# Kernel optimization log

Hardware: AMD Instinct MI355X
Metric: run time of the kernel (lower is better)

The kernel has to match this reference:

```python
import jax, jax.numpy as jnp
import numpy as np

GFD = 4096   # global feature dim (VGG fc7)
DH = 1024    # 2 * hidden_dim


def setup_inputs() -> dict:
    key = jax.random.key(0)
    ks = jax.random.split(key, 10)
    b, t_k = 32, 196
    s = lambda fan_in: 1.0 / np.sqrt(fan_in)
    return {
        "global_features": jax.random.normal(ks[0], (b, t_k, GFD), jnp.float32),
        "s_t_hat": jax.random.normal(ks[1], (b, DH), jnp.float32),
        "coverage_img": jnp.zeros((b, t_k, 1), jnp.float32),
        # params
        "Wg": jax.random.normal(ks[2], (GFD, GFD), jnp.float32) * s(GFD),
        "bg": jnp.zeros((GFD,), jnp.float32),
        "Gs": jax.random.normal(ks[3], (GFD, DH), jnp.float32) * s(GFD),
        "bgs": jnp.zeros((DH,), jnp.float32),
        "Wgs": jax.random.normal(ks[4], (DH, DH), jnp.float32) * s(DH),  # w_g_star, no bias
        "Wdec": jax.random.normal(ks[5], (DH, DH), jnp.float32) * s(DH),  # decode_proj
        "bdec": jnp.zeros((DH,), jnp.float32),
        "v": jax.random.normal(ks[6], (DH, 1), jnp.float32) * s(DH),  # score vector, no bias
    }


def reference(global_features, s_t_hat, coverage_img, Wg, bg, Gs, bgs, Wgs, Wdec, bdec, v):
    # g_star: project 4096-d region features -> 1024-d   [b, t_k, DH]
    g1 = global_features @ Wg + bg
    g_star = g1 @ Gs + bgs
    # additive (Bahdanau) scores with coverage
    w_g_star = g_star @ Wgs                       # [b, t_k, DH]
    dec_fea = s_t_hat @ Wdec + bdec               # [b, DH]
    e_a = jnp.tanh(w_g_star + dec_fea[:, None, :] + coverage_img)  # [b, t_k, DH]
    scores = e_a @ v                              # [b, t_k, 1]
    alpha_a = jax.nn.softmax(scores, axis=1)      # softmax over regions
    # attention-weighted context (the bmm)
    c_img = jnp.einsum("bt,btd->bd", alpha_a[..., 0], g_star)  # [b, DH]
    coverage_new = coverage_img + alpha_a
    return c_img, coverage_new, alpha_a
```

## Files before the change

kernel.cpp:

```cpp
#include <hip/hip_runtime.h>
#include <hip/hip_bf16.h>

typedef __attribute__((ext_vector_type(8))) short short8;
typedef __attribute__((ext_vector_type(4))) float floatx4;

#define GLOBAL_AS __attribute__((address_space(1)))
#define LDS_AS    __attribute__((address_space(3)))

__device__ __forceinline__ unsigned short f2bf_rne(float x) {
  unsigned int u = __float_as_uint(x);
  u += 0x7fffu + ((u >> 16) & 1u);
  return (unsigned short)(u >> 16);
}

__global__ void cast_f32_bf16_kernel(const float* __restrict__ in,
                                     unsigned short* __restrict__ out, int n8) {
  int i = blockIdx.x * 256 + threadIdx.x;
  if (i >= n8) return;
  const float4* p = (const float4*)in;
  float4 v0 = p[2 * i], v1 = p[2 * i + 1];
  short8 o;
  o[0] = (short)f2bf_rne(v0.x); o[1] = (short)f2bf_rne(v0.y);
  o[2] = (short)f2bf_rne(v0.z); o[3] = (short)f2bf_rne(v0.w);
  o[4] = (short)f2bf_rne(v1.x); o[5] = (short)f2bf_rne(v1.y);
  o[6] = (short)f2bf_rne(v1.z); o[7] = (short)f2bf_rne(v1.w);
  *(short8*)(out + 8 * (size_t)i) = o;
}

__global__ void transpose_cast_kernel(const float* __restrict__ in,
                                      unsigned short* __restrict__ out, int R, int C) {
  __shared__ unsigned short tile[32][33];
  int tx = threadIdx.x & 31, ty = threadIdx.x >> 5;
  int r0 = blockIdx.y * 32, c0 = blockIdx.x * 32;
#pragma unroll
  for (int j = 0; j < 32; j += 8)
    tile[ty + j][tx] = f2bf_rne(in[(size_t)(r0 + ty + j) * C + c0 + tx]);
  __syncthreads();
#pragma unroll
  for (int j = 0; j < 32; j += 8)
    out[(size_t)(c0 + ty + j) * R + r0 + tx] = tile[tx][ty + j];
}

__global__ void zero4_kernel(float* __restrict__ p, int n4) {
  int i = blockIdx.x * 256 + threadIdx.x;
  if (i < n4) ((float4*)p)[i] = make_float4(0.f, 0.f, 0.f, 0.f);
}
__global__ void init_vec_kernel(const float* __restrict__ src, float* __restrict__ dst) {
  int i = blockIdx.x * 256 + threadIdx.x;
  dst[i] = src[i];
}
__global__ void bias1_accum_kernel(const float* __restrict__ bg, const float* __restrict__ Gs,
                                   float* __restrict__ bias1) {
  int j = blockIdx.x * 256 + threadIdx.x;
  int k0 = blockIdx.y * 256;
  float acc = 0.f;
  for (int k = 0; k < 256; ++k) acc += bg[k0 + k] * Gs[(size_t)(k0 + k) * 1024 + j];
  atomicAdd(&bias1[j], acc);
}

__global__ void init_dec_kernel(const float* __restrict__ bdec, float* __restrict__ dec) {
  int i = blockIdx.x * 256 + threadIdx.x;
  dec[i] = bdec[i & 1023];
}
__global__ void dec_accum_kernel(const float* __restrict__ sth, const float* __restrict__ Wdec,
                                 float* __restrict__ dec) {
  __shared__ float ss[32][128];
  const int tid = threadIdx.x;
  const int k0 = blockIdx.y * 128;
  for (int i = tid; i < 32 * 128; i += 256) {
    int bb = i >> 7, kk = i & 127;
    ss[bb][kk] = sth[bb * 1024 + k0 + kk];
  }
  __syncthreads();
  const int j = blockIdx.x * 256 + tid;
  float acc[32];
#pragma unroll
  for (int b = 0; b < 32; ++b) acc[b] = 0.f;
  for (int kk = 0; kk < 128; ++kk) {
    float w = Wdec[(size_t)(k0 + kk) * 1024 + j];
#pragma unroll
    for (int b = 0; b < 32; ++b) acc[b] += ss[b][kk] * w;
  }
  for (int b = 0; b < 32; ++b) atomicAdd(&dec[b * 1024 + j], acc[b]);
}

template <int BM, int BN, bool HAS_BIAS, bool WRITE_F32, bool WRITE_BF16>
__global__ __launch_bounds__(256, 4) void gemm_tile_kernel(
    const unsigned short* __restrict__ A, const unsigned short* __restrict__ BT,
    const float* __restrict__ bias, float* __restrict__ Cf,
    unsigned short* __restrict__ Cb, int M, int N, int K) {
  constexpr int AF = BM / 32;
  constexpr int BF = BN / 32;
  __shared__ unsigned short lds_a[BM * 32];
  __shared__ unsigned short lds_b[BN * 32];
  const int tid = threadIdx.x;
  const int lane = tid & 63;
  const int wave = tid >> 6;
  const int wm = wave >> 1, wn = wave & 1;
  const int quad = lane >> 4, col = lane & 15;
  const int m0 = blockIdx.y * BM, n0 = blockIdx.x * BN;

  floatx4 acc[AF][BF] = {};

  const int srow = tid >> 2;
  const int skoff = (tid & 3) * 8;
  const unsigned short* a_ptr = A + (size_t)(m0 + srow) * K + skoff;
  const unsigned short* b_ptr = BT + (size_t)(n0 + srow) * K + skoff;
  const size_t rowskip = (size_t)64 * K;
  char* la_dst = (char*)lds_a + tid * 16;
  char* lb_dst = (char*)lds_b + tid * 16;

  for (int kt = 0; kt < K; kt += 32) {
    __syncthreads();
#pragma unroll
    for (int c = 0; c < BM / 64; ++c)
      __builtin_amdgcn_global_load_lds((const GLOBAL_AS void*)(a_ptr + c * rowskip),
                                       (LDS_AS void*)(la_dst + c * 4096), 16, 0, 0);
#pragma unroll
    for (int c = 0; c < BN / 64; ++c)
      __builtin_amdgcn_global_load_lds((const GLOBAL_AS void*)(b_ptr + c * rowskip),
                                       (LDS_AS void*)(lb_dst + c * 4096), 16, 0, 0);
    a_ptr += 32; b_ptr += 32;
    __syncthreads();
    short8 af[AF], bf[BF];
#pragma unroll
    for (int t = 0; t < AF; ++t)
      af[t] = *(const short8*)((const char*)lds_a + (wm * (BM / 2) + t * 16 + col) * 64 + quad * 16);
#pragma unroll
    for (int t = 0; t < BF; ++t)
      bf[t] = *(const short8*)((const char*)lds_b + (wn * (BN / 2) + t * 16 + col) * 64 + quad * 16);
#pragma unroll
    for (int tm = 0; tm < AF; ++tm)
#pragma unroll
      for (int tn = 0; tn < BF; ++tn)
        acc[tm][tn] = __builtin_amdgcn_mfma_f32_16x16x32_bf16(af[tm], bf[tn], acc[tm][tn], 0, 0, 0);
  }

#pragma unroll
  for (int tm = 0; tm < AF; ++tm) {
    const int mg = m0 + wm * (BM / 2) + tm * 16 + quad * 4;
#pragma unroll
    for (int tn = 0; tn < BF; ++tn) {
      const int ng = n0 + wn * (BN / 2) + tn * 16 + col;
      const float bv = HAS_BIAS ? bias[ng] : 0.0f;
#pragma unroll
      for (int r = 0; r < 4; ++r) {
        const float val = acc[tm][tn][r] + bv;
        if (WRITE_F32) Cf[(size_t)(mg + r) * N + ng] = val;
        if (WRITE_BF16) Cb[(size_t)(mg + r) * N + ng] = f2bf_rne(val);
      }
    }
  }
}

__global__ __launch_bounds__(256, 4) void gemm_scores_kernel(
    const unsigned short* __restrict__ A, const unsigned short* __restrict__ BT,
    const float* __restrict__ dec, const float* __restrict__ cov,
    const float* __restrict__ v, float* __restrict__ scores, int M, int N, int K) {
  __shared__ unsigned short lds_a[128 * 32];
  __shared__ unsigned short lds_b[64 * 32];
  const int tid = threadIdx.x;
  const int lane = tid & 63;
  const int wave = tid >> 6;
  const int wm = wave >> 1, wn = wave & 1;
  const int quad = lane >> 4, col = lane & 15;
  const int m0 = blockIdx.y * 128, n0 = blockIdx.x * 64;

  floatx4 acc[4][2] = {};

  const int srow = tid >> 2;
  const int skoff = (tid & 3) * 8;
  const unsigned short* a_ptr = A + (size_t)(m0 + srow) * K + skoff;
  const unsigned short* b_ptr = BT + (size_t)(n0 + srow) * K + skoff;
  const size_t rowskip = (size_t)64 * K;
  char* la_dst = (char*)lds_a + tid * 16;
  char* lb_dst = (char*)lds_b + tid * 16;

  for (int kt = 0; kt < K; kt += 32) {
    __syncthreads();
    __builtin_amdgcn_global_load_lds((const GLOBAL_AS void*)(a_ptr), (LDS_AS void*)(la_dst), 16, 0, 0);
    __builtin_amdgcn_global_load_lds((const GLOBAL_AS void*)(a_ptr + rowskip), (LDS_AS void*)(la_dst + 4096), 16, 0, 0);
    __builtin_amdgcn_global_load_lds((const GLOBAL_AS void*)(b_ptr), (LDS_AS void*)(lb_dst), 16, 0, 0);
    a_ptr += 32; b_ptr += 32;
    __syncthreads();
    short8 af[4], bf[2];
#pragma unroll
    for (int t = 0; t < 4; ++t)
      af[t] = *(const short8*)((const char*)lds_a + (wm * 64 + t * 16 + col) * 64 + quad * 16);
#pragma unroll
    for (int t = 0; t < 2; ++t)
      bf[t] = *(const short8*)((const char*)lds_b + (wn * 32 + t * 16 + col) * 64 + quad * 16);
#pragma unroll
    for (int tm = 0; tm < 4; ++tm)
#pragma unroll
      for (int tn = 0; tn < 2; ++tn)
        acc[tm][tn] = __builtin_amdgcn_mfma_f32_16x16x32_bf16(af[tm], bf[tn], acc[tm][tn], 0, 0, 0);
  }

  const int n_base = n0 + wn * 32;
  float vv[2];
#pragma unroll
  for (int tn = 0; tn < 2; ++tn) vv[tn] = v[n_base + tn * 16 + col];
#pragma unroll
  for (int tm = 0; tm < 4; ++tm) {
#pragma unroll
    for (int r = 0; r < 4; ++r) {
      const int row = m0 + wm * 64 + tm * 16 + quad * 4 + r;
      const int b = row / 196;
      const float cw = cov[row];
      const float* dr = dec + b * 1024 + n_base;
      float s = 0.f;
#pragma unroll
      for (int tn = 0; tn < 2; ++tn)
        s += tanhf(acc[tm][tn][r] + dr[tn * 16 + col] + cw) * vv[tn];
      s += __shfl_xor(s, 1, 64);
      s += __shfl_xor(s, 2, 64);
      s += __shfl_xor(s, 4, 64);
      s += __shfl_xor(s, 8, 64);
      if ((lane & 15) == 0) atomicAdd(&scores[row], s);
    }
  }
}

__global__ void softmax_kernel(const float* __restrict__ scores, const float* __restrict__ cov,
                               float* __restrict__ alpha_ws, float* __restrict__ out) {
  const int b = blockIdx.x, tid = threadIdx.x;
  const int lane = tid & 63, wid = tid >> 6;
  __shared__ float red[8];
  float s = (tid < 196) ? scores[b * 196 + tid] : -1e30f;
  float m = s;
  for (int off = 32; off > 0; off >>= 1) m = fmaxf(m, __shfl_xor(m, off, 64));
  if (lane == 0) red[wid] = m;
  __syncthreads();
  m = fmaxf(fmaxf(red[0], red[1]), fmaxf(red[2], red[3]));
  float e = (tid < 196) ? __expf(s - m) : 0.f;
  float t = e;
  for (int off = 32; off > 0; off >>= 1) t += __shfl_xor(t, off, 64);
  if (lane == 0) red[4 + wid] = t;
  __syncthreads();
  const float tot = red[4] + red[5] + red[6] + red[7];
  const float a = e / tot;
  if (tid < 196) {
    alpha_ws[b * 196 + tid] = a;
    out[32768 + b * 196 + tid] = cov[b * 196 + tid] + a;
    out[32768 + 6272 + b * 196 + tid] = a;
  }
}

__global__ __launch_bounds__(256) void ctx_kernel(const float* __restrict__ alpha,
                                                  const float* __restrict__ gstar,
                                                  float* __restrict__ out) {
  const int b = blockIdx.y;
  const int colbase = blockIdx.x * 128;
  const int c = threadIdx.x & 127;
  const int half = threadIdx.x >> 7;
  const float* g = gstar + ((size_t)b * 196 + half * 98) * 1024 + colbase + c;
  const float* al = alpha + b * 196 + half * 98;
  float acc = 0.f;
#pragma unroll 7
  for (int t = 0; t < 98; ++t) acc += al[t] * g[(size_t)t * 1024];
  __shared__ float part[256];
  part[threadIdx.x] = acc;
  __syncthreads();
  if (threadIdx.x < 128)
    out[b * 1024 + colbase + threadIdx.x] = part[threadIdx.x] + part[threadIdx.x + 128];
}

extern "C" void kernel_launch(void* const* d_in, const int* in_sizes, int n_in,
                              void* d_out, int out_size, void* d_ws, size_t ws_size,
                              hipStream_t stream) {
  (void)in_sizes; (void)n_in; (void)out_size; (void)ws_size;
  const float* gf   = (const float*)d_in[0];
  const float* sth  = (const float*)d_in[1];
  const float* cov  = (const float*)d_in[2];
  const float* Wg   = (const float*)d_in[3];
  const float* bg   = (const float*)d_in[4];
  const float* Gs   = (const float*)d_in[5];
  const float* bgs  = (const float*)d_in[6];
  const float* Wgs  = (const float*)d_in[7];
  const float* Wdec = (const float*)d_in[8];
  const float* bdec = (const float*)d_in[9];
  const float* v    = (const float*)d_in[10];
  float* out = (float*)d_out;

  char* ws = (char*)d_ws;
  unsigned short* gf_bf   = (unsigned short*)(ws + 0);
  float*          alpha   = (float*)(ws + 0);
  unsigned short* Wg_bf   = (unsigned short*)(ws + 51380224);
  float*          gstar_f = (float*)(ws + 51380224);
  unsigned short* GsT     = (unsigned short*)(ws + 84934656);
  unsigned short* WgsT    = (unsigned short*)(ws + 84934656);
  unsigned short* C1T_b   = (unsigned short*)(ws + 93323264);
  unsigned short* gstar_b = (unsigned short*)(ws + 101711872);
  float*          bias1   = (float*)(ws + 114556928);
  float*          dec     = (float*)(ws + 114561024);
  float*          scores  = (float*)(ws + 114692096);

  cast_f32_bf16_kernel<<<12544, 256, 0, stream>>>(gf, gf_bf, 3211264);
  cast_f32_bf16_kernel<<<8192, 256, 0, stream>>>(Wg, Wg_bf, 2097152);
  transpose_cast_kernel<<<dim3(32, 128), 256, 0, stream>>>(Gs, GsT, 4096, 1024);
  init_vec_kernel<<<4, 256, 0, stream>>>(bgs, bias1);
  bias1_accum_kernel<<<dim3(4, 16), 256, 0, stream>>>(bg, Gs, bias1);
  gemm_tile_kernel<128, 64, false, false, true><<<dim3(64, 8), 256, 0, stream>>>(
      GsT, Wg_bf, nullptr, nullptr, C1T_b, 1024, 4096, 4096);
  transpose_cast_kernel<<<dim3(32, 32), 256, 0, stream>>>(Wgs, WgsT, 1024, 1024);
  init_dec_kernel<<<128, 256, 0, stream>>>(bdec, dec);
  dec_accum_kernel<<<dim3(4, 8), 256, 0, stream>>>(sth, Wdec, dec);
  gemm_tile_kernel<128, 64, true, true, true><<<dim3(16, 49), 256, 0, stream>>>(
      gf_bf, C1T_b, bias1, gstar_f, gstar_b, 6272, 1024, 4096);
  zero4_kernel<<<2, 256, 0, stream>>>(scores, 392);
  gemm_scores_kernel<<<dim3(16, 49), 256, 0, stream>>>(
      gstar_b, WgsT, dec, cov, v, scores, 6272, 1024, 1024);
  softmax_kernel<<<32, 256, 0, stream>>>(scores, cov, alpha, out);
  ctx_kernel<<<dim3(8, 32), 256, 0, stream>>>(alpha, gstar_f, out);
}
```

Before: 527.8 us.

## Replace LDS-staged GEMM tiles with direct global-to-register loads and prefetch

The three GEMM kernels no longer stage tiles through LDS with global_load_lds and two barriers per k-step. Each lane now loads its MFMA fragments straight from global memory into registers and prefetches the next k-slice while the current MFMAs run. The first GEMM also moves to a smaller 64x64 tile on a larger grid. This removes the barriers and LDS traffic, but it gives up data sharing inside a block, so every wave reads its own operands from L2/HBM with 16-byte strided row accesses.

After: 989.8 us. 1.88x slower.

```diff
diff --git a/kernel.cpp b/kernel.cpp
--- a/kernel.cpp
+++ b/kernel.cpp
@@ -3,9 +3,6 @@
 
 typedef __attribute__((ext_vector_type(8))) short short8;
 typedef __attribute__((ext_vector_type(4))) float floatx4;
-
-#define GLOBAL_AS __attribute__((address_space(1)))
-#define LDS_AS    __attribute__((address_space(3)))
 
 __device__ __forceinline__ unsigned short f2bf_rne(float x) {
   unsigned int u = __float_as_uint(x);
@@ -84,64 +81,53 @@
   for (int b = 0; b < 32; ++b) atomicAdd(&dec[b * 1024 + j], acc[b]);
 }
 
-template <int BM, int BN, bool HAS_BIAS, bool WRITE_F32, bool WRITE_BF16>
-__global__ __launch_bounds__(256, 4) void gemm_tile_kernel(
+template <int AF, int BF, bool HAS_BIAS, bool WRITE_F32, bool WRITE_BF16>
+__global__ __launch_bounds__(256, 4) void gemm_flat_kernel(
     const unsigned short* __restrict__ A, const unsigned short* __restrict__ BT,
     const float* __restrict__ bias, float* __restrict__ Cf,
     unsigned short* __restrict__ Cb, int M, int N, int K) {
-  constexpr int AF = BM / 32;
-  constexpr int BF = BN / 32;
-  __shared__ unsigned short lds_a[BM * 32];
-  __shared__ unsigned short lds_b[BN * 32];
   const int tid = threadIdx.x;
   const int lane = tid & 63;
   const int wave = tid >> 6;
   const int wm = wave >> 1, wn = wave & 1;
   const int quad = lane >> 4, col = lane & 15;
-  const int m0 = blockIdx.y * BM, n0 = blockIdx.x * BN;
+  const int m0 = blockIdx.y * (32 * AF), n0 = blockIdx.x * (32 * BF);
 
   floatx4 acc[AF][BF] = {};
-
-  const int srow = tid >> 2;
-  const int skoff = (tid & 3) * 8;
-  const unsigned short* a_ptr = A + (size_t)(m0 + srow) * K + skoff;
-  const unsigned short* b_ptr = BT + (size_t)(n0 + srow) * K + skoff;
-  const size_t rowskip = (size_t)64 * K;
-  char* la_dst = (char*)lds_a + tid * 16;
-  char* lb_dst = (char*)lds_b + tid * 16;
+  const size_t K16 = (size_t)16 * K;
+  const unsigned short* a0 = A + (size_t)(m0 + wm * 16 * AF + col) * K + quad * 8;
+  const unsigned short* b0 = BT + (size_t)(n0 + wn * 16 * BF + col) * K + quad * 8;
+
+  short8 af[AF], bf[BF];
+#pragma unroll
+  for (int t = 0; t < AF; ++t) af[t] = *(const short8*)(a0 + t * K16);
+#pragma unroll
+  for (int t = 0; t < BF; ++t) bf[t] = *(const short8*)(b0 + t * K16);
 
   for (int kt = 0; kt < K; kt += 32) {
-    __syncthreads();
-#pragma unroll
-    for (int c = 0; c < BM / 64; ++c)
-      __builtin_amdgcn_global_load_lds((const GLOBAL_AS void*)(a_ptr + c * rowskip),
-                                       (LDS_AS void*)(la_dst + c * 4096), 16, 0, 0);
-#pragma unroll
-    for (int c = 0; c < BN / 64; ++c)
-      __builtin_amdgcn_global_load_lds((const GLOBAL_AS void*)(b_ptr + c * rowskip),
-                                       (LDS_AS void*)(lb_dst + c * 4096), 16, 0, 0);
-    a_ptr += 32; b_ptr += 32;
-    __syncthreads();
-    short8 af[AF], bf[BF];
-#pragma unroll
-    for (int t = 0; t < AF; ++t)
-      af[t] = *(const short8*)((const char*)lds_a + (wm * (BM / 2) + t * 16 + col) * 64 + quad * 16);
-#pragma unroll
-    for (int t = 0; t < BF; ++t)
-      bf[t] = *(const short8*)((const char*)lds_b + (wn * (BN / 2) + t * 16 + col) * 64 + quad * 16);
+    const int kn = (kt + 32 < K) ? kt + 32 : kt;
+    short8 afn[AF], bfn[BF];
+#pragma unroll
+    for (int t = 0; t < AF; ++t) afn[t] = *(const short8*)(a0 + kn + t * K16);
+#pragma unroll
+    for (int t = 0; t < BF; ++t) bfn[t] = *(const short8*)(b0 + kn + t * K16);
 #pragma unroll
     for (int tm = 0; tm < AF; ++tm)
 #pragma unroll
       for (int tn = 0; tn < BF; ++tn)
         acc[tm][tn] = __builtin_amdgcn_mfma_f32_16x16x32_bf16(af[tm], bf[tn], acc[tm][tn], 0, 0, 0);
+#pragma unroll
+    for (int t = 0; t < AF; ++t) af[t] = afn[t];
+#pragma unroll
+    for (int t = 0; t < BF; ++t) bf[t] = bfn[t];
   }
 
 #pragma unroll
   for (int tm = 0; tm < AF; ++tm) {
-    const int mg = m0 + wm * (BM / 2) + tm * 16 + quad * 4;
+    const int mg = m0 + wm * 16 * AF + tm * 16 + quad * 4;
 #pragma unroll
     for (int tn = 0; tn < BF; ++tn) {
-      const int ng = n0 + wn * (BN / 2) + tn * 16 + col;
+      const int ng = n0 + wn * 16 * BF + tn * 16 + col;
       const float bv = HAS_BIAS ? bias[ng] : 0.0f;
 #pragma unroll
       for (int r = 0; r < 4; ++r) {
@@ -153,12 +139,10 @@
   }
 }
 
-__global__ __launch_bounds__(256, 4) void gemm_scores_kernel(
+__global__ __launch_bounds__(256, 4) void gemm_scores_flat_kernel(
     const unsigned short* __restrict__ A, const unsigned short* __restrict__ BT,
     const float* __restrict__ dec, const float* __restrict__ cov,
     const float* __restrict__ v, float* __restrict__ scores, int M, int N, int K) {
-  __shared__ unsigned short lds_a[128 * 32];
-  __shared__ unsigned short lds_b[64 * 32];
   const int tid = threadIdx.x;
   const int lane = tid & 63;
   const int wave = tid >> 6;
@@ -167,34 +151,32 @@
   const int m0 = blockIdx.y * 128, n0 = blockIdx.x * 64;
 
   floatx4 acc[4][2] = {};
-
-  const int srow = tid >> 2;
-  const int skoff = (tid & 3) * 8;
-  const unsigned short* a_ptr = A + (size_t)(m0 + srow) * K + skoff;
-  const unsigned short* b_ptr = BT + (size_t)(n0 + srow) * K + skoff;
-  const size_t rowskip = (size_t)64 * K;
-  char* la_dst = (char*)lds_a + tid * 16;
-  char* lb_dst = (char*)lds_b + tid * 16;
+  const size_t K16 = (size_t)16 * K;
+  const unsigned short* a0 = A + (size_t)(m0 + wm * 64 + col) * K + quad * 8;
+  const unsigned short* b0 = BT + (size_t)(n0 + wn * 32 + col) * K + quad * 8;
+
+  short8 af[4], bf[2];
+#pragma unroll
+  for (int t = 0; t < 4; ++t) af[t] = *(const short8*)(a0 + t * K16);
+#pragma unroll
+  for (int t = 0; t < 2; ++t) bf[t] = *(const short8*)(b0 + t * K16);
 
   for (int kt = 0; kt < K; kt += 32) {
-    __syncthreads();
-    __builtin_amdgcn_global_load_lds((const GLOBAL_AS void*)(a_ptr), (LDS_AS void*)(la_dst), 16, 0, 0);
-    __builtin_amdgcn_global_load_lds((const GLOBAL_AS void*)(a_ptr + rowskip), (LDS_AS void*)(la_dst + 4096), 16, 0, 0);
-    __builtin_amdgcn_global_load_lds((const GLOBAL_AS void*)(b_ptr), (LDS_AS void*)(lb_dst), 16, 0, 0);
-    a_ptr += 32; b_ptr += 32;
-    __syncthreads();
-    short8 af[4], bf[2];
-#pragma unroll
-    for (int t = 0; t < 4; ++t)
-      af[t] = *(const short8*)((const char*)lds_a + (wm * 64 + t * 16 + col) * 64 + quad * 16);
-#pragma unroll
-    for (int t = 0; t < 2; ++t)
-      bf[t] = *(const short8*)((const char*)lds_b + (wn * 32 + t * 16 + col) * 64 + quad * 16);
+    const int kn = (kt + 32 < K) ? kt + 32 : kt;
+    short8 afn[4], bfn[2];
+#pragma unroll
+    for (int t = 0; t < 4; ++t) afn[t] = *(const short8*)(a0 + kn + t * K16);
+#pragma unroll
+    for (int t = 0; t < 2; ++t) bfn[t] = *(const short8*)(b0 + kn + t * K16);
 #pragma unroll
     for (int tm = 0; tm < 4; ++tm)
 #pragma unroll
       for (int tn = 0; tn < 2; ++tn)
         acc[tm][tn] = __builtin_amdgcn_mfma_f32_16x16x32_bf16(af[tm], bf[tn], acc[tm][tn], 0, 0, 0);
+#pragma unroll
+    for (int t = 0; t < 4; ++t) af[t] = afn[t];
+#pragma unroll
+    for (int t = 0; t < 2; ++t) bf[t] = bfn[t];
   }
 
   const int n_base = n0 + wn * 32;
@@ -301,15 +283,15 @@
   transpose_cast_kernel<<<dim3(32, 128), 256, 0, stream>>>(Gs, GsT, 4096, 1024);
   init_vec_kernel<<<4, 256, 0, stream>>>(bgs, bias1);
   bias1_accum_kernel<<<dim3(4, 16), 256, 0, stream>>>(bg, Gs, bias1);
-  gemm_tile_kernel<128, 64, false, false, true><<<dim3(64, 8), 256, 0, stream>>>(
+  gemm_flat_kernel<2, 2, false, false, true><<<dim3(64, 16), 256, 0, stream>>>(
       GsT, Wg_bf, nullptr, nullptr, C1T_b, 1024, 4096, 4096);
   transpose_cast_kernel<<<dim3(32, 32), 256, 0, stream>>>(Wgs, WgsT, 1024, 1024);
   init_dec_kernel<<<128, 256, 0, stream>>>(bdec, dec);
   dec_accum_kernel<<<dim3(4, 8), 256, 0, stream>>>(sth, Wdec, dec);
-  gemm_tile_kernel<128, 64, true, true, true><<<dim3(16, 49), 256, 0, stream>>>(
+  gemm_flat_kernel<4, 2, true, true, true><<<dim3(16, 49), 256, 0, stream>>>(
       gf_bf, C1T_b, bias1, gstar_f, gstar_b, 6272, 1024, 4096);
   zero4_kernel<<<2, 256, 0, stream>>>(scores, 392);
-  gemm_scores_kernel<<<dim3(16, 49), 256, 0, stream>>>(
+  gemm_scores_flat_kernel<<<dim3(16, 49), 256, 0, stream>>>(
       gstar_b, WgsT, dec, cov, v, scores, 6272, 1024, 1024);
   softmax_kernel<<<32, 256, 0, stream>>>(scores, cov, alpha, out);
   ctx_kernel<<<dim3(8, 32), 256, 0, stream>>>(alpha, gstar_f, out);
```
